# Optimization experiments

Hardware: AMD Instinct MI355X
Metric: run time of the kernel (lower is better)

The kernel has to match this reference:

```python
import jax, jax.numpy as jnp
import numpy as np

EMBED = 1024
MLP = 2048
N_EXPERTS = 8
TOP_K = 2


def setup_inputs() -> dict:
    key = jax.random.key(0)
    ks = jax.random.split(key, 5)
    scale_e = 1.0 / np.sqrt(EMBED)
    scale_m = 1.0 / np.sqrt(MLP)
    x = jax.random.normal(ks[0], (4, 2048, EMBED), dtype=jnp.float32)
    gate_w = jax.random.normal(ks[1], (EMBED, N_EXPERTS), dtype=jnp.float32) * scale_e
    w1 = jax.random.normal(ks[2], (N_EXPERTS, EMBED, MLP), dtype=jnp.float32) * scale_e
    w3 = jax.random.normal(ks[3], (N_EXPERTS, EMBED, MLP), dtype=jnp.float32) * scale_e
    w2 = jax.random.normal(ks[4], (N_EXPERTS, MLP, EMBED), dtype=jnp.float32) * scale_m
    return {"x": x, "gate_w": gate_w, "w1": w1, "w2": w2, "w3": w3}


def reference(x, gate_w, w1, w2, w3):
    B, S, D = x.shape
    xf = x.reshape(-1, D)  # [T, D] tokens
    # Router: softmax over experts, top-k select, renormalize selected weights
    router_logits = xf @ gate_w                      # [T, E]
    routing_weights = jax.nn.softmax(router_logits, axis=-1)
    sel_w, sel_e = jax.lax.top_k(routing_weights, TOP_K)  # [T, K]
    sel_w = sel_w / jnp.sum(sel_w, axis=-1, keepdims=True)
    out = jnp.zeros_like(xf)
    # Loop over the small fixed expert set; tokens not routed to expert e get
    # coefficient 0, matching the gather/scatter-add combine of the original.
    for e in range(N_EXPERTS):
        coef = jnp.sum(jnp.where(sel_e == e, sel_w, 0.0), axis=-1)  # [T]
        h = jax.nn.silu(xf @ w1[e]) * (xf @ w3[e])                  # [T, Mlp] SwiGLU
        out = out + coef[:, None] * (h @ w2[e])                     # [T, D]
    return out.reshape(B, S, D)
```

## Files before the change

### kernel.cpp

```cpp
#include <hip/hip_runtime.h>

#define EMBED 1024
#define MLP   2048
#define NE    8
#define NTOK  8192
#define RMAX  (2*NTOK + NE*256)

typedef _Float16 f16x8 __attribute__((ext_vector_type(8)));
typedef _Float16 f16x4 __attribute__((ext_vector_type(4)));
typedef float    f32x4 __attribute__((ext_vector_type(4)));

__device__ __forceinline__ void async_copy16(const void* g, void* l) {
  __builtin_amdgcn_global_load_lds(
      (const __attribute__((address_space(1))) unsigned int*)g,
      (__attribute__((address_space(3))) unsigned int*)l, 16, 0, 0);
}

__global__ __launch_bounds__(256) void router_kernel(
    const float* __restrict__ x, const float* __restrict__ gw,
    int* __restrict__ sel_e, float* __restrict__ sel_w, int* __restrict__ counts)
{
  __shared__ float gwt[NE * EMBED];
  __shared__ int cnt[NE];
  int tid = threadIdx.x;
  for (int idx = tid; idx < NE * EMBED; idx += 256) {
    int i = idx >> 3, e = idx & 7;
    gwt[e * EMBED + i] = gw[idx];
  }
  if (tid < NE) cnt[tid] = 0;
  __syncthreads();

  int lane = tid & 63, wv = tid >> 6;
  int t = blockIdx.x * 4 + wv;
  const float4* xr = (const float4*)(x + (size_t)t * EMBED);
  const float4* gt4 = (const float4*)gwt;
  float acc[NE];
  #pragma unroll
  for (int e = 0; e < NE; ++e) acc[e] = 0.f;
  #pragma unroll
  for (int c = 0; c < 4; ++c) {
    float4 xv = xr[c * 64 + lane];
    #pragma unroll
    for (int e = 0; e < NE; ++e) {
      float4 gv = gt4[e * 256 + c * 64 + lane];
      acc[e] += xv.x * gv.x + xv.y * gv.y + xv.z * gv.z + xv.w * gv.w;
    }
  }
  #pragma unroll
  for (int off = 1; off < 64; off <<= 1) {
    #pragma unroll
    for (int e = 0; e < NE; ++e) acc[e] += __shfl_xor(acc[e], off);
  }
  if (lane == 0) {
    int e0 = 0; float l0 = acc[0];
    #pragma unroll
    for (int e = 1; e < NE; ++e) if (acc[e] > l0) { l0 = acc[e]; e0 = e; }
    int e1 = -1; float l1 = -1e30f;
    #pragma unroll
    for (int e = 0; e < NE; ++e) if (e != e0 && acc[e] > l1) { l1 = acc[e]; e1 = e; }
    float w0 = 1.f / (1.f + expf(l1 - l0));
    sel_e[2 * t] = e0;     sel_w[2 * t] = w0;
    sel_e[2 * t + 1] = e1; sel_w[2 * t + 1] = 1.f - w0;
    atomicAdd(&cnt[e0], 1); atomicAdd(&cnt[e1], 1);
  }
  __syncthreads();
  if (tid < NE && cnt[tid]) atomicAdd(&counts[tid], cnt[tid]);
}

__global__ __launch_bounds__(256) void assign_kernel(
    const int* __restrict__ sel_e, const float* __restrict__ sel_w,
    const int* __restrict__ counts, int* __restrict__ cursor,
    int* __restrict__ offs_out, int* __restrict__ rowtok,
    float* __restrict__ rowcoef, int* __restrict__ inv)
{
  int offl[NE];
  {
    int o = 0;
    #pragma unroll
    for (int e = 0; e < NE; ++e) { offl[e] = o; o += (counts[e] + 255) & ~255; }
    if (blockIdx.x == 0 && threadIdx.x == 0) {
      #pragma unroll
      for (int e = 0; e < NE; ++e) offs_out[e] = offl[e];
      offs_out[NE] = o;
    }
  }
  int t = blockIdx.x * 256 + threadIdx.x;
  int lane = threadIdx.x & 63;
  #pragma unroll
  for (int k = 0; k < 2; ++k) {
    int e = sel_e[2 * t + k];
    float w = sel_w[2 * t + k];
    for (int xch = 0; xch < NE; ++xch) {
      unsigned long long m = __ballot(e == xch);
      if (e == xch) {
        int leader = __ffsll((unsigned long long)m) - 1;
        int base = 0;
        if (lane == leader) base = atomicAdd(&cursor[xch], (int)__popcll(m));
        base = __shfl(base, leader);
        int pos = offl[xch] + base + (int)__popcll(m & ((1ull << lane) - 1));
        rowtok[pos] = t;
        rowcoef[pos] = w;
        inv[2 * t + k] = pos;
      }
    }
  }
}

__global__ __launch_bounds__(256) void gather_kernel(
    const float* __restrict__ x, const int* __restrict__ rowtok,
    _Float16* __restrict__ xg)
{
  int r = blockIdx.x;
  int tok = rowtok[r];
  int t4 = threadIdx.x * 4;
  _Float16* dst = xg + (size_t)r * EMBED + t4;
  if (tok >= 0) {
    float4 v = *(const float4*)(x + (size_t)tok * EMBED + t4);
    f16x4 h; h.x = (_Float16)v.x; h.y = (_Float16)v.y; h.z = (_Float16)v.z; h.w = (_Float16)v.w;
    *(f16x4*)dst = h;
  } else {
    f16x4 z = {(_Float16)0.f, (_Float16)0.f, (_Float16)0.f, (_Float16)0.f};
    *(f16x4*)dst = z;
  }
}

__global__ __launch_bounds__(256) void transpose_all_kernel(
    const float* __restrict__ w1, const float* __restrict__ w3,
    const float* __restrict__ w2, _Float16* __restrict__ w1t,
    _Float16* __restrict__ w3t, _Float16* __restrict__ w2t)
{
  int id = blockIdx.x;
  int mat = id >> 12;
  int rr = id & 4095;
  int e = rr >> 9, tile = rr & 511;
  const float* src; _Float16* dst; int K, N;
  if (mat == 0)      { src = w1; dst = w1t; K = EMBED; N = MLP; }
  else if (mat == 1) { src = w3; dst = w3t; K = EMBED; N = MLP; }
  else               { src = w2; dst = w2t; K = MLP;   N = EMBED; }
  int nx = K >> 6;
  int k0 = (tile % nx) * 64, n0 = (tile / nx) * 64;
  src += (size_t)e * K * N;
  dst += (size_t)e * K * N;

  __shared__ float tilebuf[64][65];
  int t = threadIdx.x;
  int r = t >> 4, c4 = (t & 15) * 4;
  #pragma unroll
  for (int i = 0; i < 4; ++i) {
    float4 v = *(const float4*)(src + (size_t)(k0 + r + 16 * i) * N + n0 + c4);
    tilebuf[r + 16 * i][c4 + 0] = v.x;
    tilebuf[r + 16 * i][c4 + 1] = v.y;
    tilebuf[r + 16 * i][c4 + 2] = v.z;
    tilebuf[r + 16 * i][c4 + 3] = v.w;
  }
  __syncthreads();
  int kk8 = (t & 7) * 8, nIdx = t >> 3;
  #pragma unroll
  for (int i = 0; i < 2; ++i) {
    int n = nIdx + 32 * i;
    f16x8 h;
    #pragma unroll
    for (int j = 0; j < 8; ++j) h[j] = (_Float16)tilebuf[kk8 + j][n];
    *(f16x8*)(dst + (size_t)(n0 + n) * K + k0 + kk8) = h;
  }
}

__device__ __forceinline__ int resolve_expert(const int* __restrict__ offs, int r0)
{
  int e = 0;
  #pragma unroll
  for (int q = 0; q < NE - 1; ++q) if (r0 >= offs[q + 1]) e = q + 1;
  return e;
}

__device__ __forceinline__ const _Float16* frag_addr(const _Float16* buf, int row, int quad)
{
  return buf + row * 32 + ((quad ^ ((row >> 1) & 3)) << 3);
}

__global__ __launch_bounds__(512, 2) void gemm1_kernel(
    const _Float16* __restrict__ xg, const _Float16* __restrict__ w1t,
    const _Float16* __restrict__ w3t, const float* __restrict__ rowcoef,
    const int* __restrict__ offs, _Float16* __restrict__ hb)
{
  int r0 = blockIdx.x * 256;
  if (r0 >= offs[NE]) return;
  int e = resolve_expert(offs, r0);
  int n0 = blockIdx.y * 128;
  const _Float16* B1 = w1t + (size_t)e * MLP * EMBED;
  const _Float16* B3 = w3t + (size_t)e * MLP * EMBED;

  __shared__ __align__(16) _Float16 As[3][256 * 32];
  __shared__ __align__(16) _Float16 Bs1[3][128 * 32];
  __shared__ __align__(16) _Float16 Bs3[3][128 * 32];

  int tid = threadIdx.x, lane = tid & 63, wv = tid >> 6;
  int wm = (wv & 3) << 6, wn = (wv >> 2) << 6;
  int l16 = lane & 15, quad = lane >> 4;

  int rowA0 = tid >> 2, kqpA = tid & 3;
  int rowA1 = rowA0 + 128;
  int kqlA0 = kqpA ^ ((rowA0 >> 1) & 3);
  int kqlA1 = kqpA ^ ((rowA1 >> 1) & 3);
  int rowB = tid >> 2, kqpB = tid & 3;
  int kqlB = kqpB ^ ((rowB >> 1) & 3);
  size_t gA0 = (size_t)(r0 + rowA0) * EMBED + kqlA0 * 8;
  size_t gA1 = (size_t)(r0 + rowA1) * EMBED + kqlA1 * 8;
  size_t gB  = (size_t)(n0 + rowB) * EMBED + kqlB * 8;
  int lofA0 = (wv * 64) * 8;
  int lofA1 = (512 + wv * 64) * 8;
  int lofB  = (wv * 64) * 8;

  f32x4 acc1[4][4], acc3[4][4];
  f32x4 z4 = {0.f, 0.f, 0.f, 0.f};
  #pragma unroll
  for (int i = 0; i < 4; ++i)
    #pragma unroll
    for (int j = 0; j < 4; ++j) { acc1[i][j] = z4; acc3[i][j] = z4; }

  auto stage = [&](int b, int kk) {
    async_copy16(xg + gA0 + kk, &As[b][lofA0]);
    async_copy16(xg + gA1 + kk, &As[b][lofA1]);
    async_copy16(B1 + gB  + kk, &Bs1[b][lofB]);
    async_copy16(B3 + gB  + kk, &Bs3[b][lofB]);
  };

  const int NIT = EMBED / 32;
  stage(0, 0);
  for (int k = 0; k < NIT; ++k) {
    int b = k % 3;
    if (k + 1 < NIT) {
      stage((k + 1) % 3, (k + 1) * 32);
      asm volatile("s_waitcnt vmcnt(4)" ::: "memory");
    } else {
      asm volatile("s_waitcnt vmcnt(0)" ::: "memory");
    }
    asm volatile("s_barrier" ::: "memory");

    f16x8 af[4], b1f[4], b3f[4];
    #pragma unroll
    for (int i = 0; i < 4; ++i)
      af[i] = *(const f16x8*)frag_addr(As[b], wm + 16 * i + l16, quad);
    #pragma unroll
    for (int j = 0; j < 4; ++j) {
      b1f[j] = *(const f16x8*)frag_addr(Bs1[b], wn + 16 * j + l16, quad);
      b3f[j] = *(const f16x8*)frag_addr(Bs3[b], wn + 16 * j + l16, quad);
    }
    #pragma unroll
    for (int i = 0; i < 4; ++i)
      #pragma unroll
      for (int j = 0; j < 4; ++j) {
        acc1[i][j] = __builtin_amdgcn_mfma_f32_16x16x32_f16(af[i], b1f[j], acc1[i][j], 0, 0, 0);
        acc3[i][j] = __builtin_amdgcn_mfma_f32_16x16x32_f16(af[i], b3f[j], acc3[i][j], 0, 0, 0);
      }
  }

  #pragma unroll
  for (int i = 0; i < 4; ++i) {
    int mb = r0 + wm + 16 * i + quad * 4;
    float cf[4];
    #pragma unroll
    for (int rg = 0; rg < 4; ++rg) cf[rg] = rowcoef[mb + rg];
    #pragma unroll
    for (int j = 0; j < 4; ++j) {
      int col = n0 + wn + 16 * j + l16;
      #pragma unroll
      for (int rg = 0; rg < 4; ++rg) {
        float g = acc1[i][j][rg], u = acc3[i][j][rg];
        float h = g * u * cf[rg] / (1.f + __expf(-g));
        hb[(size_t)(mb + rg) * MLP + col] = (_Float16)h;
      }
    }
  }
}

__global__ __launch_bounds__(512, 2) void gemm2_kernel(
    const _Float16* __restrict__ hb, const _Float16* __restrict__ w2t,
    const int* __restrict__ offs, _Float16* __restrict__ hb2)
{
  int r0 = blockIdx.x * 256;
  if (r0 >= offs[NE]) return;
  int e = resolve_expert(offs, r0);
  int n0 = blockIdx.y * 128;
  const _Float16* B = w2t + (size_t)e * EMBED * MLP;

  __shared__ __align__(16) _Float16 As[3][256 * 32];
  __shared__ __align__(16) _Float16 Bs[3][128 * 32];

  int tid = threadIdx.x, lane = tid & 63, wv = tid >> 6;
  int wm = (wv & 3) << 6, wn = (wv >> 2) << 6;
  int l16 = lane & 15, quad = lane >> 4;

  int rowA0 = tid >> 2, kqpA = tid & 3;
  int rowA1 = rowA0 + 128;
  int kqlA0 = kqpA ^ ((rowA0 >> 1) & 3);
  int kqlA1 = kqpA ^ ((rowA1 >> 1) & 3);
  int rowB = tid >> 2, kqpB = tid & 3;
  int kqlB = kqpB ^ ((rowB >> 1) & 3);
  size_t gA0 = (size_t)(r0 + rowA0) * MLP + kqlA0 * 8;
  size_t gA1 = (size_t)(r0 + rowA1) * MLP + kqlA1 * 8;
  size_t gB  = (size_t)(n0 + rowB) * MLP + kqlB * 8;
  int lofA0 = (wv * 64) * 8;
  int lofA1 = (512 + wv * 64) * 8;
  int lofB  = (wv * 64) * 8;

  f32x4 acc[4][4];
  f32x4 z4 = {0.f, 0.f, 0.f, 0.f};
  #pragma unroll
  for (int i = 0; i < 4; ++i)
    #pragma unroll
    for (int j = 0; j < 4; ++j) acc[i][j] = z4;

  auto stage = [&](int b, int kk) {
    async_copy16(hb + gA0 + kk, &As[b][lofA0]);
    async_copy16(hb + gA1 + kk, &As[b][lofA1]);
    async_copy16(B  + gB  + kk, &Bs[b][lofB]);
  };

  const int NIT = MLP / 32;
  stage(0, 0);
  for (int k = 0; k < NIT; ++k) {
    int b = k % 3;
    if (k + 1 < NIT) {
      stage((k + 1) % 3, (k + 1) * 32);
      asm volatile("s_waitcnt vmcnt(3)" ::: "memory");
    } else {
      asm volatile("s_waitcnt vmcnt(0)" ::: "memory");
    }
    asm volatile("s_barrier" ::: "memory");

    f16x8 af[4], bf[4];
    #pragma unroll
    for (int i = 0; i < 4; ++i)
      af[i] = *(const f16x8*)frag_addr(As[b], wm + 16 * i + l16, quad);
    #pragma unroll
    for (int j = 0; j < 4; ++j)
      bf[j] = *(const f16x8*)frag_addr(Bs[b], wn + 16 * j + l16, quad);
    #pragma unroll
    for (int i = 0; i < 4; ++i)
      #pragma unroll
      for (int j = 0; j < 4; ++j)
        acc[i][j] = __builtin_amdgcn_mfma_f32_16x16x32_f16(af[i], bf[j], acc[i][j], 0, 0, 0);
  }

  #pragma unroll
  for (int i = 0; i < 4; ++i) {
    int mb = r0 + wm + 16 * i + quad * 4;
    #pragma unroll
    for (int j = 0; j < 4; ++j) {
      int col = n0 + wn + 16 * j + l16;
      #pragma unroll
      for (int rg = 0; rg < 4; ++rg)
        hb2[(size_t)(mb + rg) * EMBED + col] = (_Float16)acc[i][j][rg];
    }
  }
}

__global__ __launch_bounds__(256) void combine_kernel(
    const _Float16* __restrict__ hb2, const int* __restrict__ inv,
    float* __restrict__ out)
{
  int t = blockIdx.x;
  int d = threadIdx.x * 4;
  int p0 = inv[2 * t], p1 = inv[2 * t + 1];
  f16x4 a = *(const f16x4*)(hb2 + (size_t)p0 * EMBED + d);
  f16x4 b = *(const f16x4*)(hb2 + (size_t)p1 * EMBED + d);
  float4 r;
  r.x = (float)a.x + (float)b.x;
  r.y = (float)a.y + (float)b.y;
  r.z = (float)a.z + (float)b.z;
  r.w = (float)a.w + (float)b.w;
  *(float4*)(out + (size_t)t * EMBED + d) = r;
}

extern "C" void kernel_launch(void* const* d_in, const int* in_sizes, int n_in,
                              void* d_out, int out_size, void* d_ws, size_t ws_size,
                              hipStream_t stream)
{
  (void)in_sizes; (void)n_in; (void)ws_size; (void)out_size;
  const float* x  = (const float*)d_in[0];
  const float* gw = (const float*)d_in[1];
  const float* w1 = (const float*)d_in[2];
  const float* w2 = (const float*)d_in[3];
  const float* w3 = (const float*)d_in[4];
  float* out = (float*)d_out;
  char* ws = (char*)d_ws;

  size_t o = 0;
  auto alloc = [&](size_t bytes) { size_t r = o; o = (o + bytes + 255) & ~255ULL; return r; };
  const size_t wbytes = (size_t)NE * MLP * EMBED * 2;
  _Float16* w1t = (_Float16*)(ws + alloc(wbytes));
  _Float16* w3t = (_Float16*)(ws + alloc(wbytes));
  _Float16* w2t = (_Float16*)(ws + alloc(wbytes));
  _Float16* xg  = (_Float16*)(ws + alloc((size_t)RMAX * EMBED * 2));
  _Float16* hb  = (_Float16*)(ws + alloc((size_t)RMAX * MLP * 2));
  int*   rowtok  = (int*)(ws + alloc((size_t)RMAX * 4));
  float* rowcoef = (float*)(ws + alloc((size_t)RMAX * 4));
  int*   sel_e   = (int*)(ws + alloc((size_t)2 * NTOK * 4));
  float* sel_w   = (float*)(ws + alloc((size_t)2 * NTOK * 4));
  int*   inv     = (int*)(ws + alloc((size_t)2 * NTOK * 4));
  int*   meta    = (int*)(ws + alloc(256));
  int* counts = meta;
  int* offs   = meta + 8;
  int* cursor = meta + 17;
  _Float16* hb2 = xg;

  hipMemsetAsync(meta, 0, 256, stream);
  hipMemsetAsync(rowtok, 0xFF, (size_t)RMAX * 4, stream);
  hipMemsetAsync(rowcoef, 0, (size_t)RMAX * 4, stream);

  transpose_all_kernel<<<3 * 4096, 256, 0, stream>>>(w1, w3, w2, w1t, w3t, w2t);

  router_kernel<<<NTOK / 4, 256, 0, stream>>>(x, gw, sel_e, sel_w, counts);
  assign_kernel<<<NTOK / 256, 256, 0, stream>>>(sel_e, sel_w, counts, cursor,
                                                offs, rowtok, rowcoef, inv);
  gather_kernel<<<RMAX, 256, 0, stream>>>(x, rowtok, xg);

  gemm1_kernel<<<dim3(RMAX / 256, MLP / 128), 512, 0, stream>>>(xg, w1t, w3t, rowcoef, offs, hb);
  gemm2_kernel<<<dim3(RMAX / 256, EMBED / 128), 512, 0, stream>>>(hb, w2t, offs, hb2);
  combine_kernel<<<NTOK, 256, 0, stream>>>(hb2, inv, out);
}
```

Measured before the change: 625.3 us.

## Switch GEMMs to double-buffered LDS, raise occupancy, swizzle blocks across XCDs

```diff
diff --git a/kernel.cpp b/kernel.cpp
--- a/kernel.cpp
+++ b/kernel.cpp
@@ -178,21 +178,30 @@
   return buf + row * 32 + ((quad ^ ((row >> 1) & 3)) << 3);
 }
 
-__global__ __launch_bounds__(512, 2) void gemm1_kernel(
+__device__ __forceinline__ void swz_block(int& x, int& y)
+{
+  int lin = blockIdx.y * 72 + blockIdx.x;
+  int xcd = lin & 7, idx = lin >> 3;
+  x = xcd * 9 + idx % 9;
+  y = idx / 9;
+}
+
+__global__ __launch_bounds__(512, 4) void gemm1_kernel(
     const _Float16* __restrict__ xg, const _Float16* __restrict__ w1t,
     const _Float16* __restrict__ w3t, const float* __restrict__ rowcoef,
     const int* __restrict__ offs, _Float16* __restrict__ hb)
 {
-  int r0 = blockIdx.x * 256;
+  int bx, by; swz_block(bx, by);
+  int r0 = bx * 256;
   if (r0 >= offs[NE]) return;
   int e = resolve_expert(offs, r0);
-  int n0 = blockIdx.y * 128;
+  int n0 = by * 128;
   const _Float16* B1 = w1t + (size_t)e * MLP * EMBED;
   const _Float16* B3 = w3t + (size_t)e * MLP * EMBED;
 
-  __shared__ __align__(16) _Float16 As[3][256 * 32];
-  __shared__ __align__(16) _Float16 Bs1[3][128 * 32];
-  __shared__ __align__(16) _Float16 Bs3[3][128 * 32];
+  __shared__ __align__(16) _Float16 As[2][256 * 32];
+  __shared__ __align__(16) _Float16 Bs1[2][128 * 32];
+  __shared__ __align__(16) _Float16 Bs3[2][128 * 32];
 
   int tid = threadIdx.x, lane = tid & 63, wv = tid >> 6;
   int wm = (wv & 3) << 6, wn = (wv >> 2) << 6;
@@ -227,10 +236,10 @@
 
   const int NIT = EMBED / 32;
   stage(0, 0);
+  int b = 0;
   for (int k = 0; k < NIT; ++k) {
-    int b = k % 3;
     if (k + 1 < NIT) {
-      stage((k + 1) % 3, (k + 1) * 32);
+      stage(b ^ 1, (k + 1) * 32);
       asm volatile("s_waitcnt vmcnt(4)" ::: "memory");
     } else {
       asm volatile("s_waitcnt vmcnt(0)" ::: "memory");
@@ -246,6 +255,9 @@
       b1f[j] = *(const f16x8*)frag_addr(Bs1[b], wn + 16 * j + l16, quad);
       b3f[j] = *(const f16x8*)frag_addr(Bs3[b], wn + 16 * j + l16, quad);
     }
+    asm volatile("s_waitcnt lgkmcnt(0)" ::: "memory");
+    asm volatile("s_barrier" ::: "memory");
+
     #pragma unroll
     for (int i = 0; i < 4; ++i)
       #pragma unroll
@@ -253,6 +265,7 @@
         acc1[i][j] = __builtin_amdgcn_mfma_f32_16x16x32_f16(af[i], b1f[j], acc1[i][j], 0, 0, 0);
         acc3[i][j] = __builtin_amdgcn_mfma_f32_16x16x32_f16(af[i], b3f[j], acc3[i][j], 0, 0, 0);
       }
+    b ^= 1;
   }
 
   #pragma unroll
@@ -274,18 +287,19 @@
   }
 }
 
-__global__ __launch_bounds__(512, 2) void gemm2_kernel(
+__global__ __launch_bounds__(512, 4) void gemm2_kernel(
     const _Float16* __restrict__ hb, const _Float16* __restrict__ w2t,
     const int* __restrict__ offs, _Float16* __restrict__ hb2)
 {
-  int r0 = blockIdx.x * 256;
+  int bx, by; swz_block(bx, by);
+  int r0 = bx * 256;
   if (r0 >= offs[NE]) return;
   int e = resolve_expert(offs, r0);
-  int n0 = blockIdx.y * 128;
+  int n0 = by * 128;
   const _Float16* B = w2t + (size_t)e * EMBED * MLP;
 
-  __shared__ __align__(16) _Float16 As[3][256 * 32];
-  __shared__ __align__(16) _Float16 Bs[3][128 * 32];
+  __shared__ __align__(16) _Float16 As[2][256 * 32];
+  __shared__ __align__(16) _Float16 Bs[2][128 * 32];
 
   int tid = threadIdx.x, lane = tid & 63, wv = tid >> 6;
   int wm = (wv & 3) << 6, wn = (wv >> 2) << 6;
@@ -319,10 +333,10 @@
 
   const int NIT = MLP / 32;
   stage(0, 0);
+  int b = 0;
   for (int k = 0; k < NIT; ++k) {
-    int b = k % 3;
     if (k + 1 < NIT) {
-      stage((k + 1) % 3, (k + 1) * 32);
+      stage(b ^ 1, (k + 1) * 32);
       asm volatile("s_waitcnt vmcnt(3)" ::: "memory");
     } else {
       asm volatile("s_waitcnt vmcnt(0)" ::: "memory");
@@ -336,11 +350,15 @@
     #pragma unroll
     for (int j = 0; j < 4; ++j)
       bf[j] = *(const f16x8*)frag_addr(Bs[b], wn + 16 * j + l16, quad);
+    asm volatile("s_waitcnt lgkmcnt(0)" ::: "memory");
+    asm volatile("s_barrier" ::: "memory");
+
     #pragma unroll
     for (int i = 0; i < 4; ++i)
       #pragma unroll
       for (int j = 0; j < 4; ++j)
         acc[i][j] = __builtin_amdgcn_mfma_f32_16x16x32_f16(af[i], bf[j], acc[i][j], 0, 0, 0);
+    b ^= 1;
   }
 
   #pragma unroll
```

Result: slower. 1.825 ms (+191.9%).

## Shrink MoE GEMM tiles to 128x128 and add XCD-aware block swizzle

Applied to the files above, without the earlier changes.

```diff
diff --git a/kernel.cpp b/kernel.cpp
--- a/kernel.cpp
+++ b/kernel.cpp
@@ -178,38 +178,45 @@
   return buf + row * 32 + ((quad ^ ((row >> 1) & 3)) << 3);
 }
 
-__global__ __launch_bounds__(512, 2) void gemm1_kernel(
+__device__ __forceinline__ void swz_block(int& x, int& y)
+{
+  int lin = blockIdx.y * 144 + blockIdx.x;
+  int xcd = lin & 7, idx = lin >> 3;
+  x = xcd * 18 + idx % 18;
+  y = idx / 18;
+}
+
+__global__ __launch_bounds__(256, 2) void gemm1_kernel(
     const _Float16* __restrict__ xg, const _Float16* __restrict__ w1t,
     const _Float16* __restrict__ w3t, const float* __restrict__ rowcoef,
     const int* __restrict__ offs, _Float16* __restrict__ hb)
 {
-  int r0 = blockIdx.x * 256;
+  int bx, by; swz_block(bx, by);
+  int r0 = bx * 128;
   if (r0 >= offs[NE]) return;
   int e = resolve_expert(offs, r0);
-  int n0 = blockIdx.y * 128;
+  int n0 = by * 128;
   const _Float16* B1 = w1t + (size_t)e * MLP * EMBED;
   const _Float16* B3 = w3t + (size_t)e * MLP * EMBED;
 
-  __shared__ __align__(16) _Float16 As[3][256 * 32];
+  __shared__ __align__(16) _Float16 As[3][128 * 32];
   __shared__ __align__(16) _Float16 Bs1[3][128 * 32];
   __shared__ __align__(16) _Float16 Bs3[3][128 * 32];
 
   int tid = threadIdx.x, lane = tid & 63, wv = tid >> 6;
-  int wm = (wv & 3) << 6, wn = (wv >> 2) << 6;
+  int wm = (wv & 1) << 6, wn = (wv >> 1) << 6;
   int l16 = lane & 15, quad = lane >> 4;
 
-  int rowA0 = tid >> 2, kqpA = tid & 3;
-  int rowA1 = rowA0 + 128;
-  int kqlA0 = kqpA ^ ((rowA0 >> 1) & 3);
-  int kqlA1 = kqpA ^ ((rowA1 >> 1) & 3);
-  int rowB = tid >> 2, kqpB = tid & 3;
-  int kqlB = kqpB ^ ((rowB >> 1) & 3);
-  size_t gA0 = (size_t)(r0 + rowA0) * EMBED + kqlA0 * 8;
-  size_t gA1 = (size_t)(r0 + rowA1) * EMBED + kqlA1 * 8;
-  size_t gB  = (size_t)(n0 + rowB) * EMBED + kqlB * 8;
-  int lofA0 = (wv * 64) * 8;
-  int lofA1 = (512 + wv * 64) * 8;
-  int lofB  = (wv * 64) * 8;
+  int row0 = tid >> 2, kqp = tid & 3;
+  int row1 = row0 + 64;
+  int kql0 = kqp ^ ((row0 >> 1) & 3);
+  int kql1 = kqp ^ ((row1 >> 1) & 3);
+  size_t gA0 = (size_t)(r0 + row0) * EMBED + kql0 * 8;
+  size_t gA1 = (size_t)(r0 + row1) * EMBED + kql1 * 8;
+  size_t gB0 = (size_t)(n0 + row0) * EMBED + kql0 * 8;
+  size_t gB1 = (size_t)(n0 + row1) * EMBED + kql1 * 8;
+  int lof0 = (wv * 64) * 8;
+  int lof1 = (256 + wv * 64) * 8;
 
   f32x4 acc1[4][4], acc3[4][4];
   f32x4 z4 = {0.f, 0.f, 0.f, 0.f};
@@ -219,10 +226,12 @@
     for (int j = 0; j < 4; ++j) { acc1[i][j] = z4; acc3[i][j] = z4; }
 
   auto stage = [&](int b, int kk) {
-    async_copy16(xg + gA0 + kk, &As[b][lofA0]);
-    async_copy16(xg + gA1 + kk, &As[b][lofA1]);
-    async_copy16(B1 + gB  + kk, &Bs1[b][lofB]);
-    async_copy16(B3 + gB  + kk, &Bs3[b][lofB]);
+    async_copy16(xg + gA0 + kk, &As[b][lof0]);
+    async_copy16(xg + gA1 + kk, &As[b][lof1]);
+    async_copy16(B1 + gB0 + kk, &Bs1[b][lof0]);
+    async_copy16(B1 + gB1 + kk, &Bs1[b][lof1]);
+    async_copy16(B3 + gB0 + kk, &Bs3[b][lof0]);
+    async_copy16(B3 + gB1 + kk, &Bs3[b][lof1]);
   };
 
   const int NIT = EMBED / 32;
@@ -231,7 +240,7 @@
     int b = k % 3;
     if (k + 1 < NIT) {
       stage((k + 1) % 3, (k + 1) * 32);
-      asm volatile("s_waitcnt vmcnt(4)" ::: "memory");
+      asm volatile("s_waitcnt vmcnt(6)" ::: "memory");
     } else {
       asm volatile("s_waitcnt vmcnt(0)" ::: "memory");
     }
@@ -274,35 +283,34 @@
   }
 }
 
-__global__ __launch_bounds__(512, 2) void gemm2_kernel(
+__global__ __launch_bounds__(256, 2) void gemm2_kernel(
     const _Float16* __restrict__ hb, const _Float16* __restrict__ w2t,
     const int* __restrict__ offs, _Float16* __restrict__ hb2)
 {
-  int r0 = blockIdx.x * 256;
+  int bx, by; swz_block(bx, by);
+  int r0 = bx * 128;
   if (r0 >= offs[NE]) return;
   int e = resolve_expert(offs, r0);
-  int n0 = blockIdx.y * 128;
+  int n0 = by * 128;
   const _Float16* B = w2t + (size_t)e * EMBED * MLP;
 
-  __shared__ __align__(16) _Float16 As[3][256 * 32];
+  __shared__ __align__(16) _Float16 As[3][128 * 32];
   __shared__ __align__(16) _Float16 Bs[3][128 * 32];
 
   int tid = threadIdx.x, lane = tid & 63, wv = tid >> 6;
-  int wm = (wv & 3) << 6, wn = (wv >> 2) << 6;
+  int wm = (wv & 1) << 6, wn = (wv >> 1) << 6;
   int l16 = lane & 15, quad = lane >> 4;
 
-  int rowA0 = tid >> 2, kqpA = tid & 3;
-  int rowA1 = rowA0 + 128;
-  int kqlA0 = kqpA ^ ((rowA0 >> 1) & 3);
-  int kqlA1 = kqpA ^ ((rowA1 >> 1) & 3);
-  int rowB = tid >> 2, kqpB = tid & 3;
-  int kqlB = kqpB ^ ((rowB >> 1) & 3);
-  size_t gA0 = (size_t)(r0 + rowA0) * MLP + kqlA0 * 8;
-  size_t gA1 = (size_t)(r0 + rowA1) * MLP + kqlA1 * 8;
-  size_t gB  = (size_t)(n0 + rowB) * MLP + kqlB * 8;
-  int lofA0 = (wv * 64) * 8;
-  int lofA1 = (512 + wv * 64) * 8;
-  int lofB  = (wv * 64) * 8;
+  int row0 = tid >> 2, kqp = tid & 3;
+  int row1 = row0 + 64;
+  int kql0 = kqp ^ ((row0 >> 1) & 3);
+  int kql1 = kqp ^ ((row1 >> 1) & 3);
+  size_t gA0 = (size_t)(r0 + row0) * MLP + kql0 * 8;
+  size_t gA1 = (size_t)(r0 + row1) * MLP + kql1 * 8;
+  size_t gB0 = (size_t)(n0 + row0) * MLP + kql0 * 8;
+  size_t gB1 = (size_t)(n0 + row1) * MLP + kql1 * 8;
+  int lof0 = (wv * 64) * 8;
+  int lof1 = (256 + wv * 64) * 8;
 
   f32x4 acc[4][4];
   f32x4 z4 = {0.f, 0.f, 0.f, 0.f};
@@ -312,9 +320,10 @@
     for (int j = 0; j < 4; ++j) acc[i][j] = z4;
 
   auto stage = [&](int b, int kk) {
-    async_copy16(hb + gA0 + kk, &As[b][lofA0]);
-    async_copy16(hb + gA1 + kk, &As[b][lofA1]);
-    async_copy16(B  + gB  + kk, &Bs[b][lofB]);
+    async_copy16(hb + gA0 + kk, &As[b][lof0]);
+    async_copy16(hb + gA1 + kk, &As[b][lof1]);
+    async_copy16(B  + gB0 + kk, &Bs[b][lof0]);
+    async_copy16(B  + gB1 + kk, &Bs[b][lof1]);
   };
 
   const int NIT = MLP / 32;
@@ -323,7 +332,7 @@
     int b = k % 3;
     if (k + 1 < NIT) {
       stage((k + 1) % 3, (k + 1) * 32);
-      asm volatile("s_waitcnt vmcnt(3)" ::: "memory");
+      asm volatile("s_waitcnt vmcnt(4)" ::: "memory");
     } else {
       asm volatile("s_waitcnt vmcnt(0)" ::: "memory");
     }
@@ -416,7 +425,7 @@
                                                 offs, rowtok, rowcoef, inv);
   gather_kernel<<<RMAX, 256, 0, stream>>>(x, rowtok, xg);
 
-  gemm1_kernel<<<dim3(RMAX / 256, MLP / 128), 512, 0, stream>>>(xg, w1t, w3t, rowcoef, offs, hb);
-  gemm2_kernel<<<dim3(RMAX / 256, EMBED / 128), 512, 0, stream>>>(hb, w2t, offs, hb2);
+  gemm1_kernel<<<dim3(RMAX / 128, MLP / 128), 256, 0, stream>>>(xg, w1t, w3t, rowcoef, offs, hb);
+  gemm2_kernel<<<dim3(RMAX / 128, EMBED / 128), 256, 0, stream>>>(hb, w2t, offs, hb2);
   combine_kernel<<<NTOK, 256, 0, stream>>>(hb2, inv, out);
 }
```

Measured after the change: 594.5 us. 4.9% less time.
